# Optimization experiments

Hardware: AMD Instinct MI355X
Metric: run time of the kernel (lower is better)

Reference implementation:

```python
import jax, jax.numpy as jnp
import numpy as np

CHAN = 128
IN_CHAN = 3
NB_OUT = 10
K = 2  # maxPoolKer


def affine_grid(theta, H, W):
    # theta: [C,2,3] -> grid [C,H,W,2], torch F.affine_grid align_corners=False
    xs = (2.0 * jnp.arange(W, dtype=jnp.float32) + 1.0) / W - 1.0
    ys = (2.0 * jnp.arange(H, dtype=jnp.float32) + 1.0) / H - 1.0
    gx, gy = jnp.meshgrid(xs, ys)  # [H,W]
    base = jnp.stack([gx, gy, jnp.ones_like(gx)], axis=-1)  # [H,W,3]
    return jnp.einsum('crk,hwk->chwr', theta, base)  # [...,0]=x, [...,1]=y


def grid_sample(img, grid):
    # img [M,H,W], grid [M,H,W,2]; bilinear, zeros padding, align_corners=False
    M, H, W = img.shape
    ix = ((grid[..., 0] + 1.0) * W - 1.0) * 0.5
    iy = ((grid[..., 1] + 1.0) * H - 1.0) * 0.5
    x0 = jnp.floor(ix)
    y0 = jnp.floor(iy)
    wx = ix - x0
    wy = iy - y0

    def tap(xi, yi):
        valid = (xi >= 0) & (xi <= W - 1) & (yi >= 0) & (yi <= H - 1)
        xc = jnp.clip(xi, 0, W - 1).astype(jnp.int32)
        yc = jnp.clip(yi, 0, H - 1).astype(jnp.int32)
        v = jax.vmap(lambda im, y, x: im[y, x])(img, yc, xc)
        return jnp.where(valid, v, 0.0)

    v00 = tap(x0, y0)
    v01 = tap(x0 + 1.0, y0)
    v10 = tap(x0, y0 + 1.0)
    v11 = tap(x0 + 1.0, y0 + 1.0)
    return (1.0 - wy) * ((1.0 - wx) * v00 + wx * v01) + wy * ((1.0 - wx) * v10 + wx * v11)


def geom_layer(x, geo, lin, box):
    # x [B,Ci,H,W]; lin [C,Ci]; geo,box [C,2,3]
    B, Ci, H, W = x.shape
    C = lin.shape[0]
    y = jnp.einsum('ci,bihw->bchw', lin, x)  # channel linear combine
    grid = affine_grid(geo, H, W)            # [C,H,W,2], shared across batch
    samp = jax.vmap(lambda yb: grid_sample(yb, grid))(y)  # [B,C,H,W]
    bgrid = affine_grid(box, H, W)
    boxm = grid_sample(jnp.ones((C, H, W), samp.dtype), bgrid)  # BoxPool mask
    return samp * boxm[None]


def maxpool_g(x, k):
    # MaxPool2d_G: depthwise box-filter conv -> argmax -> gather window from padded x
    B, C, H, W = x.shape
    ch, cw = H // k, W // k
    ker = jnp.ones((1, 1, ch, cw), x.dtype) / (ch + cw)
    xr = x.reshape(B * C, 1, H, W)
    conv = jax.lax.conv_general_dilated(
        xr, ker, (1, 1), [(ch // 2, ch // 2), (cw // 2, cw // 2)])
    conv = conv[:, :, :H, :W].reshape(B, C, H * W)
    argm = jnp.argmax(conv, axis=-1)
    r = argm // H  # original code uses origImgSize[0]; assumes square H==W
    c = argm % W
    padH, padW = H + H // k, W + W // k
    top = padH // 2 - H // 2
    left = padW // 2 - W // 2
    padded = jnp.zeros((B, C, padH, padW), x.dtype).at[:, :, top:top + H, left:left + W].set(x)
    r2 = r + H // (2 * k)
    c2 = c + W // (2 * k)
    ri = r2[..., None] + (jnp.arange(ch) - ch // 2)  # [B,C,ch]
    ci = c2[..., None] + (jnp.arange(cw) - cw // 2)  # [B,C,cw]
    gat = jax.vmap(jax.vmap(lambda p, rr, cc: p[rr[:, None], cc[None, :]]))(padded, ri, ci)
    return gat  # [B,C,ch,cw]


def setup_inputs() -> dict:
    key = jax.random.key(0)
    ks = jax.random.split(key, 12)
    eye = jnp.eye(3, dtype=jnp.float32)[:2]  # [2,3]
    x = jax.random.normal(ks[0], (8, IN_CHAN, 64, 64), dtype=jnp.float32)
    geo0 = eye[None] + 0.1 * jax.random.normal(ks[1], (CHAN, 2, 3), dtype=jnp.float32)
    lin0 = jax.random.uniform(ks[2], (CHAN, IN_CHAN), dtype=jnp.float32)
    box0 = eye[None] + 0.1 * jax.random.normal(ks[3], (CHAN, 2, 3), dtype=jnp.float32)
    geos = eye[None, None] + 0.1 * jax.random.normal(ks[4], (3, CHAN, 2, 3), dtype=jnp.float32)
    lins = jax.random.uniform(ks[5], (3, CHAN, CHAN), dtype=jnp.float32)
    boxes = eye[None, None] + 0.1 * jax.random.normal(ks[6], (3, CHAN, 2, 3), dtype=jnp.float32)
    bound = 1.0 / np.sqrt(CHAN)
    dense_w = jax.random.uniform(ks[7], (NB_OUT, CHAN), dtype=jnp.float32, minval=-bound, maxval=bound)
    dense_b = jax.random.uniform(ks[8], (NB_OUT,), dtype=jnp.float32, minval=-bound, maxval=bound)
    return {"x": x, "geo0": geo0, "lin0": lin0, "box0": box0,
            "geos": geos, "lins": lins, "boxes": boxes,
            "dense_w": dense_w, "dense_b": dense_b}


def reference(x, geo0, lin0, box0, geos, lins, boxes, dense_w, dense_b):
    h = geom_layer(x, geo0, lin0, box0)            # inLay: [8,128,64,64]
    h = geom_layer(h, geos[0], lins[0], boxes[0])  # layer 0
    h = maxpool_g(h, K)                            # layer 1 (maxPoolPos=1): [8,128,32,32]
    h = geom_layer(h, geos[1], lins[1], boxes[1])  # layer 2
    h = geom_layer(h, geos[2], lins[2], boxes[2])  # layer 3
    feat = h
    pooled = feat.mean(axis=-1).mean(axis=-1)      # [B,C]
    out = pooled @ dense_w.T + dense_b             # [B,nbOut]
    return out, feat
```

## Files before the change

kernel.cpp:

```cpp
#include <hip/hip_runtime.h>

#define BB 8
#define CC 128

__global__ __launch_bounds__(256) void inlay_sample_kernel(
    const float* __restrict__ x, const float* __restrict__ lin,
    const float* __restrict__ geo, const float* __restrict__ box,
    float* __restrict__ out) {
  const int H = 64, W = 64, HW = 4096;
  __shared__ __align__(16) float cp[64 * 68];
  int bc = blockIdx.x;
  int c = bc & (CC - 1);
  int b = bc >> 7;
  int tid = threadIdx.x;
  const float* xb = x + (size_t)b * 3 * HW;

  float w0 = lin[c * 3 + 0], w1 = lin[c * 3 + 1], w2 = lin[c * 3 + 2];

#pragma unroll
  for (int k = 0; k < 4; ++k) {
    int i4 = tid + k * 256;
    int base = i4 * 4;
    float4 f0 = *reinterpret_cast<const float4*>(&xb[base]);
    float4 f1 = *reinterpret_cast<const float4*>(&xb[HW + base]);
    float4 f2 = *reinterpret_cast<const float4*>(&xb[2 * HW + base]);
    float4 cv;
    cv.x = w0 * f0.x + w1 * f1.x + w2 * f2.x;
    cv.y = w0 * f0.y + w1 * f1.y + w2 * f2.y;
    cv.z = w0 * f0.z + w1 * f1.z + w2 * f2.z;
    cv.w = w0 * f0.w + w1 * f1.w + w2 * f2.w;
    int h = i4 >> 4, w = (i4 & 15) * 4;
    *reinterpret_cast<float4*>(&cp[h * 68 + w]) = cv;
  }
  __syncthreads();

  const float* g = geo + c * 6;
  const float* bx = box + c * 6;
  float g0 = g[0], g1 = g[1], g2 = g[2], g3 = g[3], g4 = g[4], g5 = g[5];
  float b0 = bx[0], b1 = bx[1], b2 = bx[2], b3 = bx[3], b4 = bx[4], b5 = bx[5];
  float* o = out + ((size_t)b * CC + c) * HW;

#pragma unroll
  for (int k = 0; k < 16; ++k) {
    int px = tid + k * 256;
    int h = px >> 6, w = px & 63;
    float xs = (2.0f * w + 1.0f) / W - 1.0f;
    float ys = (2.0f * h + 1.0f) / H - 1.0f;
    float gx = g0 * xs + g1 * ys + g2;
    float gy = g3 * xs + g4 * ys + g5;
    float ix = ((gx + 1.0f) * W - 1.0f) * 0.5f;
    float iy = ((gy + 1.0f) * H - 1.0f) * 0.5f;
    float x0 = floorf(ix), y0 = floorf(iy);
    float wx = ix - x0, wy = iy - y0;
    float v[2][2];
#pragma unroll
    for (int dy = 0; dy < 2; ++dy)
#pragma unroll
      for (int dx = 0; dx < 2; ++dx) {
        float xf = x0 + dx, yf = y0 + dy;
        bool valid = (xf >= 0.0f) && (xf <= 63.0f) && (yf >= 0.0f) && (yf <= 63.0f);
        int xi = (int)fminf(fmaxf(xf, 0.0f), 63.0f);
        int yi = (int)fminf(fmaxf(yf, 0.0f), 63.0f);
        v[dy][dx] = valid ? cp[yi * 68 + xi] : 0.0f;
      }
    float samp = (1.0f - wy) * ((1.0f - wx) * v[0][0] + wx * v[0][1]) +
                 wy * ((1.0f - wx) * v[1][0] + wx * v[1][1]);

    float bgx = b0 * xs + b1 * ys + b2;
    float bgy = b3 * xs + b4 * ys + b5;
    float bix = ((bgx + 1.0f) * W - 1.0f) * 0.5f;
    float biy = ((bgy + 1.0f) * H - 1.0f) * 0.5f;
    float bx0 = floorf(bix), by0 = floorf(biy);
    float bwx = bix - bx0, bwy = biy - by0;
    float m[2][2];
#pragma unroll
    for (int dy = 0; dy < 2; ++dy)
#pragma unroll
      for (int dx = 0; dx < 2; ++dx) {
        float xf = bx0 + dx, yf = by0 + dy;
        m[dy][dx] = ((xf >= 0.0f) && (xf <= 63.0f) && (yf >= 0.0f) && (yf <= 63.0f)) ? 1.0f : 0.0f;
      }
    float mask = (1.0f - bwy) * ((1.0f - bwx) * m[0][0] + bwx * m[0][1]) +
                 bwy * ((1.0f - bwx) * m[1][0] + bwx * m[1][1]);
    o[px] = samp * mask;
  }
}

__global__ __launch_bounds__(256) void gemm64_kernel(
    const float* __restrict__ lin, const float* __restrict__ x,
    float* __restrict__ y, int HW) {
  const int Ci = 128;
  __shared__ __align__(16) float As[16][68];
  __shared__ __align__(16) float Bs[16][64];
  int b = blockIdx.z;
  const float* xb = x + (size_t)b * Ci * HW;
  float* yb = y + (size_t)b * CC * HW;
  int tid = threadIdx.x;
  int tx = tid & 15, ty = tid >> 4;
  int row0 = blockIdx.y * 64;
  int col0 = blockIdx.x * 64;
  int m = tid >> 2, kq = (tid & 3) * 4;
  int kk = tid >> 4, n4 = (tid & 15) * 4;
  float acc[4][4] = {};
  float4 ra = *reinterpret_cast<const float4*>(&lin[(row0 + m) * Ci + kq]);
  float4 rb = *reinterpret_cast<const float4*>(&xb[(size_t)kk * HW + col0 + n4]);
  for (int k0 = 0; k0 < 128; k0 += 16) {
    __syncthreads();
    As[kq + 0][m] = ra.x; As[kq + 1][m] = ra.y; As[kq + 2][m] = ra.z; As[kq + 3][m] = ra.w;
    *reinterpret_cast<float4*>(&Bs[kk][n4]) = rb;
    __syncthreads();
    if (k0 + 16 < 128) {
      ra = *reinterpret_cast<const float4*>(&lin[(row0 + m) * Ci + k0 + 16 + kq]);
      rb = *reinterpret_cast<const float4*>(&xb[(size_t)(k0 + 16 + kk) * HW + col0 + n4]);
    }
#pragma unroll
    for (int kki = 0; kki < 16; ++kki) {
      float4 a4 = *reinterpret_cast<const float4*>(&As[kki][ty * 4]);
      float4 b4 = *reinterpret_cast<const float4*>(&Bs[kki][tx * 4]);
      float a[4] = {a4.x, a4.y, a4.z, a4.w};
      float bv[4] = {b4.x, b4.y, b4.z, b4.w};
#pragma unroll
      for (int i = 0; i < 4; i++)
#pragma unroll
        for (int j = 0; j < 4; j++) acc[i][j] += a[i] * bv[j];
    }
  }
#pragma unroll
  for (int i = 0; i < 4; i++) {
    float* yr = yb + (size_t)(row0 + ty * 4 + i) * HW + col0 + tx * 4;
    *reinterpret_cast<float4*>(yr) = make_float4(acc[i][0], acc[i][1], acc[i][2], acc[i][3]);
  }
}

__global__ __launch_bounds__(1024, 4) void sampmax_kernel(
    const float* __restrict__ y, const float* __restrict__ geo,
    const float* __restrict__ box, float* __restrict__ out) {
  __shared__ __align__(16) float sp[64 * 68];
  __shared__ __align__(16) float arena[64 * 100];
  __shared__ float wv[16];
  __shared__ int wi[16];
  __shared__ int am_s;
  float* pl = arena;
  float* cb = arena;

  int bc = blockIdx.x;
  int c = bc & (CC - 1);
  int b = bc >> 7;
  int tid = threadIdx.x;

  const float* plane = y + (size_t)bc * 4096;
  *reinterpret_cast<float4*>(&pl[tid * 4]) = *reinterpret_cast<const float4*>(&plane[tid * 4]);
  __syncthreads();

  {
    const float* g = geo + c * 6;
    const float* bx = box + c * 6;
    float g0 = g[0], g1 = g[1], g2 = g[2], g3 = g[3], g4 = g[4], g5 = g[5];
    float b0 = bx[0], b1 = bx[1], b2 = bx[2], b3 = bx[3], b4 = bx[4], b5 = bx[5];
#pragma unroll
    for (int k = 0; k < 4; ++k) {
      int px = tid + k * 1024;
      int h = px >> 6, w = px & 63;
      float xs = (2.0f * w + 1.0f) / 64.0f - 1.0f;
      float ys = (2.0f * h + 1.0f) / 64.0f - 1.0f;
      float gx = g0 * xs + g1 * ys + g2;
      float gy = g3 * xs + g4 * ys + g5;
      float ix = ((gx + 1.0f) * 64.0f - 1.0f) * 0.5f;
      float iy = ((gy + 1.0f) * 64.0f - 1.0f) * 0.5f;
      float x0 = floorf(ix), y0 = floorf(iy);
      float wx = ix - x0, wy = iy - y0;
      float v[2][2];
#pragma unroll
      for (int dy = 0; dy < 2; ++dy)
#pragma unroll
        for (int dx = 0; dx < 2; ++dx) {
          float xf = x0 + dx, yf = y0 + dy;
          bool valid = (xf >= 0.0f) && (xf <= 63.0f) && (yf >= 0.0f) && (yf <= 63.0f);
          int xi = (int)fminf(fmaxf(xf, 0.0f), 63.0f);
          int yi = (int)fminf(fmaxf(yf, 0.0f), 63.0f);
          v[dy][dx] = valid ? pl[yi * 64 + xi] : 0.0f;
        }
      float samp = (1.0f - wy) * ((1.0f - wx) * v[0][0] + wx * v[0][1]) +
                   wy * ((1.0f - wx) * v[1][0] + wx * v[1][1]);
      float bgx = b0 * xs + b1 * ys + b2;
      float bgy = b3 * xs + b4 * ys + b5;
      float bix = ((bgx + 1.0f) * 64.0f - 1.0f) * 0.5f;
      float biy = ((bgy + 1.0f) * 64.0f - 1.0f) * 0.5f;
      float bx0 = floorf(bix), by0 = floorf(biy);
      float bwx = bix - bx0, bwy = biy - by0;
      float m[2][2];
#pragma unroll
      for (int dy = 0; dy < 2; ++dy)
#pragma unroll
        for (int dx = 0; dx < 2; ++dx) {
          float xf = bx0 + dx, yf = by0 + dy;
          m[dy][dx] = ((xf >= 0.0f) && (xf <= 63.0f) && (yf >= 0.0f) && (yf <= 63.0f)) ? 1.0f : 0.0f;
        }
      float mask = (1.0f - bwy) * ((1.0f - bwx) * m[0][0] + bwx * m[0][1]) +
                   bwy * ((1.0f - bwx) * m[1][0] + bwx * m[1][1]);
      sp[h * 68 + w] = samp * mask;
    }
  }
  __syncthreads();

  if (tid < 256) {
    int strip = tid >> 4, w4 = (tid & 15) * 4;
    int h0 = strip * 4;
    float4 a0 = make_float4(0.f, 0.f, 0.f, 0.f), a1 = a0, a2 = a0, a3 = a0;
#pragma unroll
    for (int j = 0; j < 35; ++j) {
      int r = h0 + j - 16;
      bool valid = (r >= 0) && (r < 64);
      int rc = valid ? r : 0;
      float4 f = *reinterpret_cast<const float4*>(&sp[rc * 68 + w4]);
      f.x = valid ? f.x : 0.0f; f.y = valid ? f.y : 0.0f;
      f.z = valid ? f.z : 0.0f; f.w = valid ? f.w : 0.0f;
      if (j <= 31) { a0.x += f.x; a0.y += f.y; a0.z += f.z; a0.w += f.w; }
      if (j >= 1 && j <= 32) { a1.x += f.x; a1.y += f.y; a1.z += f.z; a1.w += f.w; }
      if (j >= 2 && j <= 33) { a2.x += f.x; a2.y += f.y; a2.z += f.z; a2.w += f.w; }
      if (j >= 3) { a3.x += f.x; a3.y += f.y; a3.z += f.z; a3.w += f.w; }
    }
    *reinterpret_cast<float4*>(&cb[(h0 + 0) * 100 + 16 + w4]) = a0;
    *reinterpret_cast<float4*>(&cb[(h0 + 1) * 100 + 16 + w4]) = a1;
    *reinterpret_cast<float4*>(&cb[(h0 + 2) * 100 + 16 + w4]) = a2;
    *reinterpret_cast<float4*>(&cb[(h0 + 3) * 100 + 16 + w4]) = a3;
  } else if (tid < 768) {
    int l = tid - 256;
    int row = l >> 3, gq = l & 7;
    int base = row * 100 + ((gq < 4) ? gq * 4 : 80 + (gq - 4) * 4);
    *reinterpret_cast<float4*>(&cb[base]) = make_float4(0.f, 0.f, 0.f, 0.f);
  }
  __syncthreads();

  float best = -3.402823466e+38f;
  int bidx = 0x7fffffff;
  {
    int h = tid >> 4, w4 = (tid & 15) * 4;
    float s0 = 0.f, s1 = 0.f, s2 = 0.f, s3 = 0.f;
#pragma unroll
    for (int q = 0; q < 9; ++q) {
      float4 f = *reinterpret_cast<const float4*>(&cb[h * 100 + w4 + 4 * q]);
      float fe[4] = {f.x, f.y, f.z, f.w};
#pragma unroll
      for (int e = 0; e < 4; ++e) {
        int u = 4 * q + e;
        if (u <= 31) s0 += fe[e];
        if (u >= 1 && u <= 32) s1 += fe[e];
        if (u >= 2 && u <= 33) s2 += fe[e];
        if (u >= 3 && u <= 34) s3 += fe[e];
      }
    }
    float sv[4] = {s0, s1, s2, s3};
#pragma unroll
    for (int d = 0; d < 4; ++d) {
      int i = (h << 6) + w4 + d;
      if (sv[d] > best) { best = sv[d]; bidx = i; }
    }
  }
#pragma unroll
  for (int off = 32; off > 0; off >>= 1) {
    float v2 = __shfl_down(best, off);
    int i2 = __shfl_down(bidx, off);
    if (v2 > best || (v2 == best && i2 < bidx)) { best = v2; bidx = i2; }
  }
  if ((tid & 63) == 0) { wv[tid >> 6] = best; wi[tid >> 6] = bidx; }
  __syncthreads();
  if (tid == 0) {
    float bv = wv[0]; int bi = wi[0];
#pragma unroll
    for (int k = 1; k < 16; ++k)
      if (wv[k] > bv || (wv[k] == bv && wi[k] < bi)) { bv = wv[k]; bi = wi[k]; }
    am_s = bi;
  }
  __syncthreads();

  int am = am_s;
  int r = am >> 6, cx = am & 63;
  float* o = out + (size_t)bc * 1024;
  {
    int oi = tid >> 5, oj = tid & 31;
    int rr = r + oi - 16, cj = cx + oj - 16;
    bool v = (rr >= 0) && (rr < 64) && (cj >= 0) && (cj < 64);
    int rrc = v ? rr : 0, cjc = v ? cj : 0;
    o[tid] = v ? sp[rrc * 68 + cjc] : 0.0f;
  }
}

template <bool POOL>
__global__ __launch_bounds__(256) void fused32_kernel(
    const float* __restrict__ lin, const float* __restrict__ x,
    const float* __restrict__ geo, const float* __restrict__ box,
    float* __restrict__ out, float* __restrict__ pooled) {
  const int H = 32, W = 32, HW = 1024;
  __shared__ __align__(16) float pls[2][1024];
  __shared__ float wred[8];
  int b = blockIdx.x & 7;
  int c0 = (blockIdx.x >> 3) * 2;
  int tid = threadIdx.x;
  const float* xb = x + (size_t)b * 128 * HW;
  const float* l0 = lin + (c0 + 0) * 128;
  const float* l1 = lin + (c0 + 1) * 128;
  int px4 = tid * 4;

  float4 acc0 = make_float4(0.f, 0.f, 0.f, 0.f);
  float4 acc1 = acc0;
#pragma unroll 8
  for (int k = 0; k < 128; ++k) {
    float4 xv = *reinterpret_cast<const float4*>(&xb[(size_t)k * HW + px4]);
    float s0 = l0[k], s1 = l1[k];
    acc0.x += s0 * xv.x; acc0.y += s0 * xv.y; acc0.z += s0 * xv.z; acc0.w += s0 * xv.w;
    acc1.x += s1 * xv.x; acc1.y += s1 * xv.y; acc1.z += s1 * xv.z; acc1.w += s1 * xv.w;
  }
  *reinterpret_cast<float4*>(&pls[0][px4]) = acc0;
  *reinterpret_cast<float4*>(&pls[1][px4]) = acc1;
  __syncthreads();

  float psum[2] = {0.f, 0.f};
#pragma unroll
  for (int c = 0; c < 2; ++c) {
    const float* g = geo + (c0 + c) * 6;
    const float* bxp = box + (c0 + c) * 6;
    float g0 = g[0], g1 = g[1], g2 = g[2], g3 = g[3], g4 = g[4], g5 = g[5];
    float b0 = bxp[0], b1 = bxp[1], b2 = bxp[2], b3 = bxp[3], b4 = bxp[4], b5 = bxp[5];
    float* o = out + ((size_t)b * CC + c0 + c) * HW;
    const float* pl = pls[c];
#pragma unroll
    for (int k = 0; k < 4; ++k) {
      int px = tid + k * 256;
      int h = px >> 5, w = px & 31;
      float xs = (2.0f * w + 1.0f) / W - 1.0f;
      float ys = (2.0f * h + 1.0f) / H - 1.0f;
      float gx = g0 * xs + g1 * ys + g2;
      float gy = g3 * xs + g4 * ys + g5;
      float ix = ((gx + 1.0f) * W - 1.0f) * 0.5f;
      float iy = ((gy + 1.0f) * H - 1.0f) * 0.5f;
      float x0 = floorf(ix), y0 = floorf(iy);
      float wx = ix - x0, wy = iy - y0;
      float v[2][2];
#pragma unroll
      for (int dy = 0; dy < 2; ++dy)
#pragma unroll
        for (int dx = 0; dx < 2; ++dx) {
          float xf = x0 + dx, yf = y0 + dy;
          bool valid = (xf >= 0.0f) && (xf <= 31.0f) && (yf >= 0.0f) && (yf <= 31.0f);
          int xi = (int)fminf(fmaxf(xf, 0.0f), 31.0f);
          int yi = (int)fminf(fmaxf(yf, 0.0f), 31.0f);
          v[dy][dx] = valid ? pl[yi * 32 + xi] : 0.0f;
        }
      float samp = (1.0f - wy) * ((1.0f - wx) * v[0][0] + wx * v[0][1]) +
                   wy * ((1.0f - wx) * v[1][0] + wx * v[1][1]);
      float bgx = b0 * xs + b1 * ys + b2;
      float bgy = b3 * xs + b4 * ys + b5;
      float bix = ((bgx + 1.0f) * W - 1.0f) * 0.5f;
      float biy = ((bgy + 1.0f) * H - 1.0f) * 0.5f;
      float bx0 = floorf(bix), by0 = floorf(biy);
      float bwx = bix - bx0, bwy = biy - by0;
      float m[2][2];
#pragma unroll
      for (int dy = 0; dy < 2; ++dy)
#pragma unroll
        for (int dx = 0; dx < 2; ++dx) {
          float xf = bx0 + dx, yf = by0 + dy;
          m[dy][dx] = ((xf >= 0.0f) && (xf <= 31.0f) && (yf >= 0.0f) && (yf <= 31.0f)) ? 1.0f : 0.0f;
        }
      float mask = (1.0f - bwy) * ((1.0f - bwx) * m[0][0] + bwx * m[0][1]) +
                   bwy * ((1.0f - bwx) * m[1][0] + bwx * m[1][1]);
      float res = samp * mask;
      o[px] = res;
      if (POOL) psum[c] += res;
    }
  }
  if (POOL) {
    int lane = tid & 63, wid = tid >> 6;
#pragma unroll
    for (int c = 0; c < 2; ++c) {
      float r = psum[c];
#pragma unroll
      for (int off = 32; off > 0; off >>= 1) r += __shfl_down(r, off);
      if (lane == 0) wred[c * 4 + wid] = r;
    }
    __syncthreads();
    if (tid < 2) {
      float t = wred[tid * 4] + wred[tid * 4 + 1] + wred[tid * 4 + 2] + wred[tid * 4 + 3];
      pooled[b * CC + c0 + tid] = t * (1.0f / 1024.0f);
    }
  }
}

__global__ __launch_bounds__(128) void dense_kernel(
    const float* __restrict__ pooled, const float* __restrict__ w,
    const float* __restrict__ bias, float* __restrict__ out) {
  int t = threadIdx.x;
  if (t < 80) {
    int b = t / 10, o = t % 10;
    float s = bias[o];
    const float* pb = pooled + b * 128;
    const float* wo = w + o * 128;
    for (int c = 0; c < 128; ++c) s += pb[c] * wo[c];
    out[b * 10 + o] = s;
  }
}

extern "C" void kernel_launch(void* const* d_in, const int* in_sizes, int n_in,
                              void* d_out, int out_size, void* d_ws, size_t ws_size,
                              hipStream_t stream) {
  const float* x     = (const float*)d_in[0];
  const float* geo0  = (const float*)d_in[1];
  const float* lin0  = (const float*)d_in[2];
  const float* box0  = (const float*)d_in[3];
  const float* geos  = (const float*)d_in[4];
  const float* lins  = (const float*)d_in[5];
  const float* boxes = (const float*)d_in[6];
  const float* dw    = (const float*)d_in[7];
  const float* db    = (const float*)d_in[8];

  float* out  = (float*)d_out;
  float* feat = out + 80;
  float* ws   = (float*)d_ws;
  float* ws0  = ws;
  float* ws1  = ws + 4194304;
  float* pooled = ws + 8388608;

  inlay_sample_kernel<<<dim3(BB * CC), 256, 0, stream>>>(x, lin0, geo0, box0, ws1);
  gemm64_kernel<<<dim3(64, 2, BB), 256, 0, stream>>>(lins, ws1, ws0, 4096);
  sampmax_kernel<<<dim3(BB * CC), 1024, 0, stream>>>(ws0, geos, boxes, ws1);
  fused32_kernel<false><<<dim3(512), 256, 0, stream>>>(lins + 16384, ws1, geos + 768, boxes + 768, ws0, nullptr);
  fused32_kernel<true><<<dim3(512), 256, 0, stream>>>(lins + 32768, ws0, geos + 1536, boxes + 1536, feat, pooled);
  dense_kernel<<<1, 128, 0, stream>>>(pooled, dw, db, out);
}
```

Before: 163.3 us.

## Fuse 128-channel linear combine into sampling/maxpool kernel, drop separate GEMM

Removes the tiled GEMM kernel and computes each output channel plane's linear combination inside the sampling/argmax kernel by streaming all 128 input planes per block. This eliminates one launch and the intermediate write/read of the mixed tensor. In exchange every block rereads the whole batch input, multiplying global/cache traffic by the channel count and losing GEMM-style data reuse.

```diff
diff --git a/kernel.cpp b/kernel.cpp
--- a/kernel.cpp
+++ b/kernel.cpp
@@ -86,55 +86,10 @@
   }
 }
 
-__global__ __launch_bounds__(256) void gemm64_kernel(
+__global__ __launch_bounds__(1024, 4) void fused_gsamp_kernel(
     const float* __restrict__ lin, const float* __restrict__ x,
-    float* __restrict__ y, int HW) {
-  const int Ci = 128;
-  __shared__ __align__(16) float As[16][68];
-  __shared__ __align__(16) float Bs[16][64];
-  int b = blockIdx.z;
-  const float* xb = x + (size_t)b * Ci * HW;
-  float* yb = y + (size_t)b * CC * HW;
-  int tid = threadIdx.x;
-  int tx = tid & 15, ty = tid >> 4;
-  int row0 = blockIdx.y * 64;
-  int col0 = blockIdx.x * 64;
-  int m = tid >> 2, kq = (tid & 3) * 4;
-  int kk = tid >> 4, n4 = (tid & 15) * 4;
-  float acc[4][4] = {};
-  float4 ra = *reinterpret_cast<const float4*>(&lin[(row0 + m) * Ci + kq]);
-  float4 rb = *reinterpret_cast<const float4*>(&xb[(size_t)kk * HW + col0 + n4]);
-  for (int k0 = 0; k0 < 128; k0 += 16) {
-    __syncthreads();
-    As[kq + 0][m] = ra.x; As[kq + 1][m] = ra.y; As[kq + 2][m] = ra.z; As[kq + 3][m] = ra.w;
-    *reinterpret_cast<float4*>(&Bs[kk][n4]) = rb;
-    __syncthreads();
-    if (k0 + 16 < 128) {
-      ra = *reinterpret_cast<const float4*>(&lin[(row0 + m) * Ci + k0 + 16 + kq]);
-      rb = *reinterpret_cast<const float4*>(&xb[(size_t)(k0 + 16 + kk) * HW + col0 + n4]);
-    }
-#pragma unroll
-    for (int kki = 0; kki < 16; ++kki) {
-      float4 a4 = *reinterpret_cast<const float4*>(&As[kki][ty * 4]);
-      float4 b4 = *reinterpret_cast<const float4*>(&Bs[kki][tx * 4]);
-      float a[4] = {a4.x, a4.y, a4.z, a4.w};
-      float bv[4] = {b4.x, b4.y, b4.z, b4.w};
-#pragma unroll
-      for (int i = 0; i < 4; i++)
-#pragma unroll
-        for (int j = 0; j < 4; j++) acc[i][j] += a[i] * bv[j];
-    }
-  }
-#pragma unroll
-  for (int i = 0; i < 4; i++) {
-    float* yr = yb + (size_t)(row0 + ty * 4 + i) * HW + col0 + tx * 4;
-    *reinterpret_cast<float4*>(yr) = make_float4(acc[i][0], acc[i][1], acc[i][2], acc[i][3]);
-  }
-}
-
-__global__ __launch_bounds__(1024, 4) void sampmax_kernel(
-    const float* __restrict__ y, const float* __restrict__ geo,
-    const float* __restrict__ box, float* __restrict__ out) {
+    const float* __restrict__ geo, const float* __restrict__ box,
+    float* __restrict__ out) {
   __shared__ __align__(16) float sp[64 * 68];
   __shared__ __align__(16) float arena[64 * 100];
   __shared__ float wv[16];
@@ -143,13 +98,21 @@
   float* pl = arena;
   float* cb = arena;
 
-  int bc = blockIdx.x;
-  int c = bc & (CC - 1);
-  int b = bc >> 7;
+  int b = blockIdx.x & 7;
+  int c = blockIdx.x >> 3;
   int tid = threadIdx.x;
-
-  const float* plane = y + (size_t)bc * 4096;
-  *reinterpret_cast<float4*>(&pl[tid * 4]) = *reinterpret_cast<const float4*>(&plane[tid * 4]);
+  const float* xb = x + (size_t)b * 128 * 4096;
+  const float* lc = lin + c * 128;
+  int px4 = tid * 4;
+
+  float4 acc = make_float4(0.f, 0.f, 0.f, 0.f);
+#pragma unroll 8
+  for (int k = 0; k < 128; ++k) {
+    float4 xv = *reinterpret_cast<const float4*>(&xb[(size_t)k * 4096 + px4]);
+    float s = lc[k];
+    acc.x += s * xv.x; acc.y += s * xv.y; acc.z += s * xv.z; acc.w += s * xv.w;
+  }
+  *reinterpret_cast<float4*>(&pl[px4]) = acc;
   __syncthreads();
 
   {
@@ -276,7 +239,7 @@
 
   int am = am_s;
   int r = am >> 6, cx = am & 63;
-  float* o = out + (size_t)bc * 1024;
+  float* o = out + ((size_t)b * CC + c) * 1024;
   {
     int oi = tid >> 5, oj = tid & 31;
     int rr = r + oi - 16, cj = cx + oj - 16;
@@ -422,9 +385,8 @@
   float* pooled = ws + 8388608;
 
   inlay_sample_kernel<<<dim3(BB * CC), 256, 0, stream>>>(x, lin0, geo0, box0, ws1);
-  gemm64_kernel<<<dim3(64, 2, BB), 256, 0, stream>>>(lins, ws1, ws0, 4096);
-  sampmax_kernel<<<dim3(BB * CC), 1024, 0, stream>>>(ws0, geos, boxes, ws1);
-  fused32_kernel<false><<<dim3(512), 256, 0, stream>>>(lins + 16384, ws1, geos + 768, boxes + 768, ws0, nullptr);
-  fused32_kernel<true><<<dim3(512), 256, 0, stream>>>(lins + 32768, ws0, geos + 1536, boxes + 1536, feat, pooled);
+  fused_gsamp_kernel<<<dim3(1024), 1024, 0, stream>>>(lins, ws1, geos, boxes, ws0);
+  fused32_kernel<false><<<dim3(512), 256, 0, stream>>>(lins + 16384, ws0, geos + 768, boxes + 768, ws1, nullptr);
+  fused32_kernel<true><<<dim3(512), 256, 0, stream>>>(lins + 32768, ws1, geos + 1536, boxes + 1536, feat, pooled);
   dense_kernel<<<1, 128, 0, stream>>>(pooled, dw, db, out);
 }
```

After: 205.6 us. 1.26x slower.

## Fuse input-layer sampling into the following channel GEMM as B-tile producer

Applied to the files above, without the earlier changes.

Merges the input-layer kernel (3-to-128 channel combine, bilinear sampling, box mask) with the 128x128 channel GEMM of layer 0. Each block loads the three input planes of one image into shared memory, builds the sampled B tile for one image row directly in shared memory, and multiplies it against all 128 output channels. This avoids writing and re-reading the 16 MB intermediate activation and saves one launch. In exchange it uses about 62 KB of shared memory per block, has only 512 blocks, computes three-channel combines per tap, and leaves a redundant dead load in the A-tile loop.

```diff
diff --git a/kernel.cpp b/kernel.cpp
--- a/kernel.cpp
+++ b/kernel.cpp
@@ -3,131 +3,116 @@
 #define BB 8
 #define CC 128
 
-__global__ __launch_bounds__(256) void inlay_sample_kernel(
-    const float* __restrict__ x, const float* __restrict__ lin,
-    const float* __restrict__ geo, const float* __restrict__ box,
-    float* __restrict__ out) {
-  const int H = 64, W = 64, HW = 4096;
-  __shared__ __align__(16) float cp[64 * 68];
-  int bc = blockIdx.x;
-  int c = bc & (CC - 1);
-  int b = bc >> 7;
+__global__ __launch_bounds__(256) void inlay_gemm_kernel(
+    const float* __restrict__ x, const float* __restrict__ lin0,
+    const float* __restrict__ geo0, const float* __restrict__ box0,
+    const float* __restrict__ lins, float* __restrict__ y) {
+  __shared__ __align__(16) float xpl[3][64 * 68];
+  __shared__ __align__(16) float As[16][132];
+  __shared__ __align__(16) float Bs[16][64];
+  int colt = blockIdx.x;
+  int b = blockIdx.y;
   int tid = threadIdx.x;
-  const float* xb = x + (size_t)b * 3 * HW;
-
-  float w0 = lin[c * 3 + 0], w1 = lin[c * 3 + 1], w2 = lin[c * 3 + 2];
-
-#pragma unroll
-  for (int k = 0; k < 4; ++k) {
-    int i4 = tid + k * 256;
-    int base = i4 * 4;
-    float4 f0 = *reinterpret_cast<const float4*>(&xb[base]);
-    float4 f1 = *reinterpret_cast<const float4*>(&xb[HW + base]);
-    float4 f2 = *reinterpret_cast<const float4*>(&xb[2 * HW + base]);
-    float4 cv;
-    cv.x = w0 * f0.x + w1 * f1.x + w2 * f2.x;
-    cv.y = w0 * f0.y + w1 * f1.y + w2 * f2.y;
-    cv.z = w0 * f0.z + w1 * f1.z + w2 * f2.z;
-    cv.w = w0 * f0.w + w1 * f1.w + w2 * f2.w;
-    int h = i4 >> 4, w = (i4 & 15) * 4;
-    *reinterpret_cast<float4*>(&cp[h * 68 + w]) = cv;
-  }
-  __syncthreads();
-
-  const float* g = geo + c * 6;
-  const float* bx = box + c * 6;
-  float g0 = g[0], g1 = g[1], g2 = g[2], g3 = g[3], g4 = g[4], g5 = g[5];
-  float b0 = bx[0], b1 = bx[1], b2 = bx[2], b3 = bx[3], b4 = bx[4], b5 = bx[5];
-  float* o = out + ((size_t)b * CC + c) * HW;
-
-#pragma unroll
-  for (int k = 0; k < 16; ++k) {
-    int px = tid + k * 256;
-    int h = px >> 6, w = px & 63;
-    float xs = (2.0f * w + 1.0f) / W - 1.0f;
-    float ys = (2.0f * h + 1.0f) / H - 1.0f;
-    float gx = g0 * xs + g1 * ys + g2;
-    float gy = g3 * xs + g4 * ys + g5;
-    float ix = ((gx + 1.0f) * W - 1.0f) * 0.5f;
-    float iy = ((gy + 1.0f) * H - 1.0f) * 0.5f;
-    float x0 = floorf(ix), y0 = floorf(iy);
-    float wx = ix - x0, wy = iy - y0;
-    float v[2][2];
-#pragma unroll
-    for (int dy = 0; dy < 2; ++dy)
-#pragma unroll
-      for (int dx = 0; dx < 2; ++dx) {
-        float xf = x0 + dx, yf = y0 + dy;
-        bool valid = (xf >= 0.0f) && (xf <= 63.0f) && (yf >= 0.0f) && (yf <= 63.0f);
-        int xi = (int)fminf(fmaxf(xf, 0.0f), 63.0f);
-        int yi = (int)fminf(fmaxf(yf, 0.0f), 63.0f);
-        v[dy][dx] = valid ? cp[yi * 68 + xi] : 0.0f;
-      }
-    float samp = (1.0f - wy) * ((1.0f - wx) * v[0][0] + wx * v[0][1]) +
-                 wy * ((1.0f - wx) * v[1][0] + wx * v[1][1]);
-
-    float bgx = b0 * xs + b1 * ys + b2;
-    float bgy = b3 * xs + b4 * ys + b5;
-    float bix = ((bgx + 1.0f) * W - 1.0f) * 0.5f;
-    float biy = ((bgy + 1.0f) * H - 1.0f) * 0.5f;
-    float bx0 = floorf(bix), by0 = floorf(biy);
-    float bwx = bix - bx0, bwy = biy - by0;
-    float m[2][2];
-#pragma unroll
-    for (int dy = 0; dy < 2; ++dy)
-#pragma unroll
-      for (int dx = 0; dx < 2; ++dx) {
-        float xf = bx0 + dx, yf = by0 + dy;
-        m[dy][dx] = ((xf >= 0.0f) && (xf <= 63.0f) && (yf >= 0.0f) && (yf <= 63.0f)) ? 1.0f : 0.0f;
-      }
-    float mask = (1.0f - bwy) * ((1.0f - bwx) * m[0][0] + bwx * m[0][1]) +
-                 bwy * ((1.0f - bwx) * m[1][0] + bwx * m[1][1]);
-    o[px] = samp * mask;
-  }
-}
-
-__global__ __launch_bounds__(256) void gemm64_kernel(
-    const float* __restrict__ lin, const float* __restrict__ x,
-    float* __restrict__ y, int HW) {
-  const int Ci = 128;
-  __shared__ __align__(16) float As[16][68];
-  __shared__ __align__(16) float Bs[16][64];
-  int b = blockIdx.z;
-  const float* xb = x + (size_t)b * Ci * HW;
-  float* yb = y + (size_t)b * CC * HW;
-  int tid = threadIdx.x;
-  int tx = tid & 15, ty = tid >> 4;
-  int row0 = blockIdx.y * 64;
-  int col0 = blockIdx.x * 64;
-  int m = tid >> 2, kq = (tid & 3) * 4;
-  int kk = tid >> 4, n4 = (tid & 15) * 4;
-  float acc[4][4] = {};
-  float4 ra = *reinterpret_cast<const float4*>(&lin[(row0 + m) * Ci + kq]);
-  float4 rb = *reinterpret_cast<const float4*>(&xb[(size_t)kk * HW + col0 + n4]);
+  int col0 = colt * 64;
+  const float* xb = x + (size_t)b * 3 * 4096;
+  float* yb = y + (size_t)b * CC * 4096;
+
+#pragma unroll
+  for (int q = 0; q < 12; ++q) {
+    int i4 = tid + q * 256;
+    int p = i4 >> 10;
+    int r = (i4 & 1023);
+    int h = r >> 4, w = (r & 15) * 4;
+    *reinterpret_cast<float4*>(&xpl[p][h * 68 + w]) =
+        *reinterpret_cast<const float4*>(&xb[p * 4096 + r * 4]);
+  }
+  __syncthreads();
+
+  int ty = tid >> 4, tx = tid & 15;
+  int am = tid >> 2, akq = (tid & 3) * 4;
+  float acc[8][4] = {};
+
+  const int hrow = colt;
+  const float ys = (2.0f * hrow + 1.0f) / 64.0f - 1.0f;
+
   for (int k0 = 0; k0 < 128; k0 += 16) {
     __syncthreads();
-    As[kq + 0][m] = ra.x; As[kq + 1][m] = ra.y; As[kq + 2][m] = ra.z; As[kq + 3][m] = ra.w;
-    *reinterpret_cast<float4*>(&Bs[kk][n4]) = rb;
+#pragma unroll
+    for (int q = 0; q < 2; ++q) {
+      int l = tid + q * 256;
+      int m = l >> 2;
+      float4 av = *reinterpret_cast<const float4*>(&lins[m * 128 + k0 + akq]);
+      (void)av;
+      int kq = (l & 3) * 4;
+      float4 av2 = *reinterpret_cast<const float4*>(&lins[m * 128 + k0 + kq]);
+      As[kq + 0][m] = av2.x; As[kq + 1][m] = av2.y;
+      As[kq + 2][m] = av2.z; As[kq + 3][m] = av2.w;
+    }
+#pragma unroll
+    for (int q = 0; q < 4; ++q) {
+      int l = tid + q * 256;
+      int kk = l >> 6;
+      int w = l & 63;
+      int ch = k0 + kk;
+      float w0 = lin0[ch * 3 + 0], w1 = lin0[ch * 3 + 1], w2 = lin0[ch * 3 + 2];
+      const float* g = geo0 + ch * 6;
+      const float* bx = box0 + ch * 6;
+      float xs = (2.0f * w + 1.0f) / 64.0f - 1.0f;
+      float gx = g[0] * xs + g[1] * ys + g[2];
+      float gy = g[3] * xs + g[4] * ys + g[5];
+      float ix = ((gx + 1.0f) * 64.0f - 1.0f) * 0.5f;
+      float iy = ((gy + 1.0f) * 64.0f - 1.0f) * 0.5f;
+      float x0 = floorf(ix), y0 = floorf(iy);
+      float wx = ix - x0, wy = iy - y0;
+      float v[2][2];
+#pragma unroll
+      for (int dy = 0; dy < 2; ++dy)
+#pragma unroll
+        for (int dx = 0; dx < 2; ++dx) {
+          float xf = x0 + dx, yf = y0 + dy;
+          bool valid = (xf >= 0.0f) && (xf <= 63.0f) && (yf >= 0.0f) && (yf <= 63.0f);
+          int xi = (int)fminf(fmaxf(xf, 0.0f), 63.0f);
+          int yi = (int)fminf(fmaxf(yf, 0.0f), 63.0f);
+          int t = yi * 68 + xi;
+          float vv = w0 * xpl[0][t] + w1 * xpl[1][t] + w2 * xpl[2][t];
+          v[dy][dx] = valid ? vv : 0.0f;
+        }
+      float samp = (1.0f - wy) * ((1.0f - wx) * v[0][0] + wx * v[0][1]) +
+                   wy * ((1.0f - wx) * v[1][0] + wx * v[1][1]);
+      float bgx = bx[0] * xs + bx[1] * ys + bx[2];
+      float bgy = bx[3] * xs + bx[4] * ys + bx[5];
+      float bix = ((bgx + 1.0f) * 64.0f - 1.0f) * 0.5f;
+      float biy = ((bgy + 1.0f) * 64.0f - 1.0f) * 0.5f;
+      float bx0 = floorf(bix), by0 = floorf(biy);
+      float bwx = bix - bx0, bwy = biy - by0;
+      float m[2][2];
+#pragma unroll
+      for (int dy = 0; dy < 2; ++dy)
+#pragma unroll
+        for (int dx = 0; dx < 2; ++dx) {
+          float xf = bx0 + dx, yf = by0 + dy;
+          m[dy][dx] = ((xf >= 0.0f) && (xf <= 63.0f) && (yf >= 0.0f) && (yf <= 63.0f)) ? 1.0f : 0.0f;
+        }
+      float mask = (1.0f - bwy) * ((1.0f - bwx) * m[0][0] + bwx * m[0][1]) +
+                   bwy * ((1.0f - bwx) * m[1][0] + bwx * m[1][1]);
+      Bs[kk][w] = samp * mask;
+    }
     __syncthreads();
-    if (k0 + 16 < 128) {
-      ra = *reinterpret_cast<const float4*>(&lin[(row0 + m) * Ci + k0 + 16 + kq]);
-      rb = *reinterpret_cast<const float4*>(&xb[(size_t)(k0 + 16 + kk) * HW + col0 + n4]);
-    }
 #pragma unroll
     for (int kki = 0; kki < 16; ++kki) {
-      float4 a4 = *reinterpret_cast<const float4*>(&As[kki][ty * 4]);
-      float4 b4 = *reinterpret_cast<const float4*>(&Bs[kki][tx * 4]);
-      float a[4] = {a4.x, a4.y, a4.z, a4.w};
-      float bv[4] = {b4.x, b4.y, b4.z, b4.w};
-#pragma unroll
-      for (int i = 0; i < 4; i++)
+      float a[8], bv[4];
+      *reinterpret_cast<float4*>(&a[0]) = *reinterpret_cast<const float4*>(&As[kki][ty * 8]);
+      *reinterpret_cast<float4*>(&a[4]) = *reinterpret_cast<const float4*>(&As[kki][ty * 8 + 4]);
+      *reinterpret_cast<float4*>(&bv[0]) = *reinterpret_cast<const float4*>(&Bs[kki][tx * 4]);
+#pragma unroll
+      for (int i = 0; i < 8; i++)
 #pragma unroll
         for (int j = 0; j < 4; j++) acc[i][j] += a[i] * bv[j];
     }
   }
 #pragma unroll
-  for (int i = 0; i < 4; i++) {
-    float* yr = yb + (size_t)(row0 + ty * 4 + i) * HW + col0 + tx * 4;
+  for (int i = 0; i < 8; i++) {
+    float* yr = yb + (size_t)(ty * 8 + i) * 4096 + col0 + tx * 4;
     *reinterpret_cast<float4*>(yr) = make_float4(acc[i][0], acc[i][1], acc[i][2], acc[i][3]);
   }
 }
@@ -421,8 +406,7 @@
   float* ws1  = ws + 4194304;
   float* pooled = ws + 8388608;
 
-  inlay_sample_kernel<<<dim3(BB * CC), 256, 0, stream>>>(x, lin0, geo0, box0, ws1);
-  gemm64_kernel<<<dim3(64, 2, BB), 256, 0, stream>>>(lins, ws1, ws0, 4096);
+  inlay_gemm_kernel<<<dim3(64, BB), 256, 0, stream>>>(x, lin0, geo0, box0, lins, ws0);
   sampmax_kernel<<<dim3(BB * CC), 1024, 0, stream>>>(ws0, geos, boxes, ws1);
   fused32_kernel<false><<<dim3(512), 256, 0, stream>>>(lins + 16384, ws1, geos + 768, boxes + 768, ws0, nullptr);
   fused32_kernel<true><<<dim3(512), 256, 0, stream>>>(lins + 32768, ws0, geos + 1536, boxes + 1536, feat, pooled);
```

After: 184.4 us. +12.9%, slower.

## Split channel reduction across two thread halves and spread box-filter column sums

Applied to the files above, without the earlier changes.

fused32_kernel now runs 512 threads per block. The two halves each reduce 64 of the 128 input channels and combine their partial sums through shared memory, and the sampling loop and pooled-sum reduction are adjusted to match. The aim is more memory-level parallelism on the latency-bound channel-combine loop, at the cost of an extra barrier and more shared memory. In sampmax, the vertical box-filter pass now gives every thread one output row instead of using 256 threads with register sliding over 4 rows. This spreads the work across all 1024 threads but performs redundant shared-memory loads (32 per output instead of about 35 per 4 outputs).

```diff
diff --git a/kernel.cpp b/kernel.cpp
--- a/kernel.cpp
+++ b/kernel.cpp
@@ -203,32 +203,25 @@
   }
   __syncthreads();
 
-  if (tid < 256) {
-    int strip = tid >> 4, w4 = (tid & 15) * 4;
-    int h0 = strip * 4;
-    float4 a0 = make_float4(0.f, 0.f, 0.f, 0.f), a1 = a0, a2 = a0, a3 = a0;
-#pragma unroll
-    for (int j = 0; j < 35; ++j) {
-      int r = h0 + j - 16;
+  {
+    int h = tid >> 4, w4 = (tid & 15) * 4;
+    float4 a = make_float4(0.f, 0.f, 0.f, 0.f);
+#pragma unroll
+    for (int j = 0; j < 32; ++j) {
+      int r = h + j - 16;
       bool valid = (r >= 0) && (r < 64);
       int rc = valid ? r : 0;
       float4 f = *reinterpret_cast<const float4*>(&sp[rc * 68 + w4]);
       f.x = valid ? f.x : 0.0f; f.y = valid ? f.y : 0.0f;
       f.z = valid ? f.z : 0.0f; f.w = valid ? f.w : 0.0f;
-      if (j <= 31) { a0.x += f.x; a0.y += f.y; a0.z += f.z; a0.w += f.w; }
-      if (j >= 1 && j <= 32) { a1.x += f.x; a1.y += f.y; a1.z += f.z; a1.w += f.w; }
-      if (j >= 2 && j <= 33) { a2.x += f.x; a2.y += f.y; a2.z += f.z; a2.w += f.w; }
-      if (j >= 3) { a3.x += f.x; a3.y += f.y; a3.z += f.z; a3.w += f.w; }
-    }
-    *reinterpret_cast<float4*>(&cb[(h0 + 0) * 100 + 16 + w4]) = a0;
-    *reinterpret_cast<float4*>(&cb[(h0 + 1) * 100 + 16 + w4]) = a1;
-    *reinterpret_cast<float4*>(&cb[(h0 + 2) * 100 + 16 + w4]) = a2;
-    *reinterpret_cast<float4*>(&cb[(h0 + 3) * 100 + 16 + w4]) = a3;
-  } else if (tid < 768) {
-    int l = tid - 256;
-    int row = l >> 3, gq = l & 7;
-    int base = row * 100 + ((gq < 4) ? gq * 4 : 80 + (gq - 4) * 4);
-    *reinterpret_cast<float4*>(&cb[base]) = make_float4(0.f, 0.f, 0.f, 0.f);
+      a.x += f.x; a.y += f.y; a.z += f.z; a.w += f.w;
+    }
+    *reinterpret_cast<float4*>(&cb[h * 100 + 16 + w4]) = a;
+    if (tid < 512) {
+      int row = tid >> 3, gq = tid & 7;
+      int base = row * 100 + ((gq < 4) ? gq * 4 : 80 + (gq - 4) * 4);
+      *reinterpret_cast<float4*>(&cb[base]) = make_float4(0.f, 0.f, 0.f, 0.f);
+    }
   }
   __syncthreads();
 
@@ -287,32 +280,48 @@
 }
 
 template <bool POOL>
-__global__ __launch_bounds__(256) void fused32_kernel(
+__global__ __launch_bounds__(512) void fused32_kernel(
     const float* __restrict__ lin, const float* __restrict__ x,
     const float* __restrict__ geo, const float* __restrict__ box,
     float* __restrict__ out, float* __restrict__ pooled) {
   const int H = 32, W = 32, HW = 1024;
   __shared__ __align__(16) float pls[2][1024];
-  __shared__ float wred[8];
+  __shared__ __align__(16) float part[2][1024];
+  __shared__ float wred[16];
   int b = blockIdx.x & 7;
   int c0 = (blockIdx.x >> 3) * 2;
   int tid = threadIdx.x;
+  int g4 = tid & 255;
+  int half = tid >> 8;
   const float* xb = x + (size_t)b * 128 * HW;
   const float* l0 = lin + (c0 + 0) * 128;
   const float* l1 = lin + (c0 + 1) * 128;
-  int px4 = tid * 4;
+  int px4 = g4 * 4;
 
   float4 acc0 = make_float4(0.f, 0.f, 0.f, 0.f);
   float4 acc1 = acc0;
+  int kb = half * 64;
 #pragma unroll 8
-  for (int k = 0; k < 128; ++k) {
+  for (int kk = 0; kk < 64; ++kk) {
+    int k = kb + kk;
     float4 xv = *reinterpret_cast<const float4*>(&xb[(size_t)k * HW + px4]);
     float s0 = l0[k], s1 = l1[k];
     acc0.x += s0 * xv.x; acc0.y += s0 * xv.y; acc0.z += s0 * xv.z; acc0.w += s0 * xv.w;
     acc1.x += s1 * xv.x; acc1.y += s1 * xv.y; acc1.z += s1 * xv.z; acc1.w += s1 * xv.w;
   }
-  *reinterpret_cast<float4*>(&pls[0][px4]) = acc0;
-  *reinterpret_cast<float4*>(&pls[1][px4]) = acc1;
+  if (half == 1) {
+    *reinterpret_cast<float4*>(&part[0][px4]) = acc0;
+    *reinterpret_cast<float4*>(&part[1][px4]) = acc1;
+  }
+  __syncthreads();
+  if (half == 0) {
+    float4 p0 = *reinterpret_cast<const float4*>(&part[0][px4]);
+    float4 p1 = *reinterpret_cast<const float4*>(&part[1][px4]);
+    acc0.x += p0.x; acc0.y += p0.y; acc0.z += p0.z; acc0.w += p0.w;
+    acc1.x += p1.x; acc1.y += p1.y; acc1.z += p1.z; acc1.w += p1.w;
+    *reinterpret_cast<float4*>(&pls[0][px4]) = acc0;
+    *reinterpret_cast<float4*>(&pls[1][px4]) = acc1;
+  }
   __syncthreads();
 
   float psum[2] = {0.f, 0.f};
@@ -325,8 +334,8 @@
     float* o = out + ((size_t)b * CC + c0 + c) * HW;
     const float* pl = pls[c];
 #pragma unroll
-    for (int k = 0; k < 4; ++k) {
-      int px = tid + k * 256;
+    for (int k = 0; k < 2; ++k) {
+      int px = tid + k * 512;
       int h = px >> 5, w = px & 31;
       float xs = (2.0f * w + 1.0f) / W - 1.0f;
       float ys = (2.0f * h + 1.0f) / H - 1.0f;
@@ -377,11 +386,13 @@
       float r = psum[c];
 #pragma unroll
       for (int off = 32; off > 0; off >>= 1) r += __shfl_down(r, off);
-      if (lane == 0) wred[c * 4 + wid] = r;
+      if (lane == 0) wred[c * 8 + wid] = r;
     }
     __syncthreads();
     if (tid < 2) {
-      float t = wred[tid * 4] + wred[tid * 4 + 1] + wred[tid * 4 + 2] + wred[tid * 4 + 3];
+      float t = 0.0f;
+#pragma unroll
+      for (int wdx = 0; wdx < 8; ++wdx) t += wred[tid * 8 + wdx];
       pooled[b * CC + c0 + tid] = t * (1.0f / 1024.0f);
     }
   }
@@ -424,7 +435,7 @@
   inlay_sample_kernel<<<dim3(BB * CC), 256, 0, stream>>>(x, lin0, geo0, box0, ws1);
   gemm64_kernel<<<dim3(64, 2, BB), 256, 0, stream>>>(lins, ws1, ws0, 4096);
   sampmax_kernel<<<dim3(BB * CC), 1024, 0, stream>>>(ws0, geos, boxes, ws1);
-  fused32_kernel<false><<<dim3(512), 256, 0, stream>>>(lins + 16384, ws1, geos + 768, boxes + 768, ws0, nullptr);
-  fused32_kernel<true><<<dim3(512), 256, 0, stream>>>(lins + 32768, ws0, geos + 1536, boxes + 1536, feat, pooled);
+  fused32_kernel<false><<<dim3(512), 512, 0, stream>>>(lins + 16384, ws1, geos + 768, boxes + 768, ws0, nullptr);
+  fused32_kernel<true><<<dim3(512), 512, 0, stream>>>(lins + 32768, ws0, geos + 1536, boxes + 1536, feat, pooled);
   dense_kernel<<<1, 128, 0, stream>>>(pooled, dw, db, out);
 }
```

After: 170.9 us. +4.6%, slower.
